# Optimization experiments

Hardware: AMD Instinct MI355X
Metric: run time of the kernel (lower is better)

The kernel has to match this reference:

```python
import jax, jax.numpy as jnp
import numpy as np

B, S, D, DH = 2, 2048, 1024, 64
H = D // DH
EPS = 1e-6

def rms_norm(x):
    # flax RMSNorm, use_scale=False: x / sqrt(mean(x^2) + eps)
    return x * jax.lax.rsqrt(jnp.mean(jnp.square(x), axis=-1, keepdims=True) + EPS)

def setup_inputs() -> dict:
    key = jax.random.key(0)
    ks = jax.random.split(key, 6)
    std = (1.0 / D) ** 0.5
    x = jax.random.normal(ks[0], (B, S, D), dtype=jnp.float32)
    Wq = jax.random.normal(ks[1], (D, D), dtype=jnp.float32) * std
    Wk = jax.random.normal(ks[2], (D, D), dtype=jnp.float32) * std
    Wv = jax.random.normal(ks[3], (D, D), dtype=jnp.float32) * std
    # output_proj is zero-initialized in the original; use small random so
    # backward through it is non-trivial for kernel correctness testing.
    Wo = jax.random.normal(ks[4], (D, D), dtype=jnp.float32) * std
    mask = jnp.tril(jnp.ones((S, S), dtype=bool))[None, None]  # causal [1,1,S,S]
    return {"x": x, "Wq": Wq, "Wk": Wk, "Wv": Wv, "Wo": Wo, "mask": mask}

def reference(x, Wq, Wk, Wv, Wo, mask):
    scale = (1.0 / DH) ** 0.5
    q = (x @ Wq).reshape(B, S, H, DH).transpose(0, 2, 1, 3)  # [B,H,S,DH]
    k = (x @ Wk).reshape(B, S, H, DH).transpose(0, 2, 1, 3)
    v = (x @ Wv).reshape(B, S, H, DH).transpose(0, 2, 1, 3)
    q = rms_norm(q)
    k = rms_norm(k)
    scores = jnp.einsum('bhsd,bhtd->bhst', q, k) * scale
    scores = jnp.where(mask, scores, jnp.finfo(scores.dtype).min)
    probs = jax.nn.softmax(scores, axis=-1)
    out = jnp.einsum('bhst,bhtd->bhsd', probs, v)
    out = out.transpose(0, 2, 1, 3).reshape(B, S, D)
    return out @ Wo
```

## Files before the change

### kernel.cpp

```cpp
#include <hip/hip_runtime.h>
#include <stdint.h>


typedef __attribute__((ext_vector_type(8))) short s16x8;
typedef __attribute__((ext_vector_type(4))) float fx4;
typedef __attribute__((ext_vector_type(4))) unsigned int ux4;
typedef __attribute__((ext_vector_type(2))) unsigned int ux2;

__device__ __forceinline__ unsigned short f2bf(float x) {
  unsigned u = __builtin_bit_cast(unsigned, x);
  u += 0x7fffu + ((u >> 16) & 1u);
  return (unsigned short)(u >> 16);
}
__device__ __forceinline__ float bf2f(unsigned short h) {
  return __builtin_bit_cast(float, (unsigned)h << 16);
}

__device__ __forceinline__ void gload_lds16(const void* g, void* l) {
  __builtin_amdgcn_global_load_lds(
      (const __attribute__((address_space(1))) unsigned int*)g,
      (__attribute__((address_space(3))) unsigned int*)l, 16, 0, 0);
}

__global__ void k_conv_bf16(const float* __restrict__ X,
                            unsigned short* __restrict__ Y, int n4) {
  int stride = gridDim.x * blockDim.x;
  for (int i = blockIdx.x * blockDim.x + threadIdx.x; i < n4; i += stride) {
    fx4 v = *(const fx4*)(X + (size_t)i * 4);
    ux2 o;
    o[0] = (unsigned)f2bf(v[0]) | ((unsigned)f2bf(v[1]) << 16);
    o[1] = (unsigned)f2bf(v[2]) | ((unsigned)f2bf(v[3]) << 16);
    *(ux2*)(Y + (size_t)i * 4) = o;
  }
}

__global__ void k_transpose_w(const float* __restrict__ W0, const float* __restrict__ W1,
                              const float* __restrict__ W2, const float* __restrict__ W3,
                              unsigned short* __restrict__ T0, unsigned short* __restrict__ T1,
                              unsigned short* __restrict__ T2, unsigned short* __restrict__ T3) {
  const float* W = blockIdx.z == 0 ? W0 : blockIdx.z == 1 ? W1 : blockIdx.z == 2 ? W2 : W3;
  unsigned short* T = blockIdx.z == 0 ? T0 : blockIdx.z == 1 ? T1 : blockIdx.z == 2 ? T2 : T3;
  __shared__ float t[32][33];
  int bx = blockIdx.x * 32, by = blockIdx.y * 32;
  int tx = threadIdx.x, ty = threadIdx.y;
#pragma unroll
  for (int i = 0; i < 32; i += 8)
    t[ty + i][tx] = W[(size_t)(by + ty + i) * 1024 + bx + tx];
  __syncthreads();
#pragma unroll
  for (int i = 0; i < 32; i += 8)
    T[(size_t)(bx + ty + i) * 1024 + by + tx] = f2bf(t[tx][ty + i]);
}

template <int MODE>
__global__ __launch_bounds__(256, 2)
void k_gemm_bt(const unsigned short* __restrict__ A,
               const unsigned short* __restrict__ W0,
               const unsigned short* __restrict__ W1,
               const unsigned short* __restrict__ W2,
               void* __restrict__ Cptr, int ldc,
               unsigned short* __restrict__ qn, unsigned short* __restrict__ kn,
               unsigned short* __restrict__ vb) {
  __shared__ unsigned short As[128 * 64];
  __shared__ unsigned short Bs[128 * 64];
  const int tid = threadIdx.x;
  const int w = tid >> 6, l = tid & 63;
  const int lr = l & 15, lg = l >> 4;
  const int wm = w >> 1, wn = w & 1;
  const int m0 = blockIdx.x * 128;
  const int nt = blockIdx.y;
  const unsigned short* Bt = (nt < 8) ? W0 : (nt < 16) ? W1 : W2;
  const int n0 = (nt & 7) * 128;

  fx4 acc[4][4] = {};

  const int srow = w * 8 + (l >> 3);
  const int skb  = ((l & 7) ^ (l >> 3)) * 8;
  const unsigned short* aB = A  + (size_t)(m0 + srow) * 1024 + skb;
  const unsigned short* bB = Bt + (size_t)(n0 + srow) * 1024 + skb;
  unsigned short* aD = &As[w * 512];
  unsigned short* bD = &Bs[w * 512];
  const int rdswz = (l & 7) << 4;

  for (int kt = 0; kt < 1024; kt += 64) {
    __syncthreads();
#pragma unroll
    for (int j = 0; j < 4; ++j) {
      gload_lds16(aB + j * 32768 + kt, aD + j * 2048);
      gload_lds16(bB + j * 32768 + kt, bD + j * 2048);
    }
    __syncthreads();
#pragma unroll
    for (int ks = 0; ks < 2; ++ks) {
      const int kb = (ks * 64 + lg * 16) ^ rdswz;
      s16x8 af[4], bf[4];
#pragma unroll
      for (int mf = 0; mf < 4; ++mf)
        af[mf] = *(const s16x8*)((const char*)As + (wm * 64 + mf * 16 + lr) * 128 + kb);
#pragma unroll
      for (int nf = 0; nf < 4; ++nf)
        bf[nf] = *(const s16x8*)((const char*)Bs + (wn * 64 + nf * 16 + lr) * 128 + kb);
#pragma unroll
      for (int mf = 0; mf < 4; ++mf)
#pragma unroll
        for (int nf = 0; nf < 4; ++nf)
          acc[mf][nf] = __builtin_amdgcn_mfma_f32_16x16x32_bf16(af[mf], bf[nf], acc[mf][nf], 0, 0, 0);
    }
  }

  if (MODE == 1) {
    const int gn = nt * 128 + wn * 64;
    const int gm = m0 + wm * 64;
#pragma unroll
    for (int mf = 0; mf < 4; ++mf)
#pragma unroll
      for (int r = 0; r < 4; ++r) {
        int row = gm + mf * 16 + lg * 4 + r;
        float* C = (float*)Cptr + (size_t)row * ldc + gn;
#pragma unroll
        for (int nf = 0; nf < 4; ++nf) C[nf * 16 + lr] = acc[mf][nf][r];
      }
  } else {
    const int tz = nt >> 3;
    const int h  = ((nt & 7) << 1) | wn;
    const int gm = m0 + wm * 64;
    unsigned short* base = tz == 0 ? qn : tz == 1 ? kn : vb;
    const float cmul = (tz == 0) ? 0.18033688f : 1.0f;
#pragma unroll
    for (int mf = 0; mf < 4; ++mf)
#pragma unroll
      for (int r = 0; r < 4; ++r) {
        int m = gm + mf * 16 + lg * 4 + r;
        float ss = 0.f;
#pragma unroll
        for (int nf = 0; nf < 4; ++nf) ss += acc[mf][nf][r] * acc[mf][nf][r];
        ss += __shfl_xor(ss, 1);
        ss += __shfl_xor(ss, 2);
        ss += __shfl_xor(ss, 4);
        ss += __shfl_xor(ss, 8);
        float scale = (tz == 2) ? 1.0f : rsqrtf(ss * (1.0f / 64.0f) + 1e-6f) * cmul;
        int b = m >> 11, s = m & 2047;
        unsigned short* dst = base + ((size_t)(((b << 4) + h) * 2048 + s)) * 64;
#pragma unroll
        for (int nf = 0; nf < 4; ++nf)
          dst[nf * 16 + lr] = f2bf(acc[mf][nf][r] * scale);
      }
  }
}

__global__ __launch_bounds__(256, 2)
void k_attn(const unsigned short* __restrict__ Q,
            const unsigned short* __restrict__ K,
            const unsigned short* __restrict__ V,
            unsigned short* __restrict__ O) {
  __shared__ unsigned short Ks[2][64 * 64];
  __shared__ unsigned short Vt[2][64 * 64];
  __shared__ unsigned short Ps[4][32 * 64];

  const int id = blockIdx.x;
  const int bh = id & 31;
  const int traw = id >> 5;
  const int tq = (traw < 8) ? traw : 23 - traw;
  const int q0 = tq * 128;
  const int tid = threadIdx.x;
  const int w = tid >> 6, l = tid & 63;
  const int lr = l & 15, lg = l >> 4;
  const int b = bh >> 4, h = bh & 15;
  const int qw = q0 + w * 32;

  const unsigned short* Kb = K + (size_t)bh * 2048 * 64;
  const unsigned short* Vb = V + (size_t)bh * 2048 * 64;
  const unsigned short* Qb = Q + ((size_t)bh * 2048 + qw) * 64;

  s16x8 aq[2][2];
#pragma unroll
  for (int mf = 0; mf < 2; ++mf)
#pragma unroll
    for (int ks = 0; ks < 2; ++ks)
      aq[mf][ks] = *(const s16x8*)(Qb + (mf * 16 + lr) * 64 + ks * 32 + lg * 8);

  fx4 oacc[2][4] = {};
  float lsum[2][4] = {{0.f, 0.f, 0.f, 0.f}, {0.f, 0.f, 0.f, 0.f}};

  const int ksrow = w * 8 + (l >> 3);
  const int kskb = ((l & 7) ^ (l >> 3)) * 8;
  const int vhalf = (tid & 31) >> 4;
  const int va_   = tid & 15;
  const int vdhg  = tid >> 5;
  const int vr0   = vhalf * 32 + va_;
  const int rdswz = (lr & 7) << 4;
  const float FMAX = 11.5415603f;

  const int ntl = 2 * (tq + 1);

  ux4 va0, va1;
#pragma unroll
  for (int j = 0; j < 2; ++j)
    gload_lds16(Kb + (size_t)(j * 32 + ksrow) * 64 + kskb, &Ks[0][j * 2048 + w * 512]);
  va0 = *(const ux4*)(Vb + (size_t)vr0 * 64 + vdhg * 8);
  va1 = *(const ux4*)(Vb + (size_t)(vr0 + 16) * 64 + vdhg * 8);
  {
    union { ux4 v; unsigned short u[8]; } a0, a1;
    a0.v = va0; a1.v = va1;
#pragma unroll
    for (int i = 0; i < 8; ++i) {
      int dh = vdhg * 8 + i;
      *(unsigned*)((char*)&Vt[0][0] + dh * 128 + ((vhalf * 64 + va_ * 4) ^ (i << 4))) =
          (unsigned)a0.u[i] | ((unsigned)a1.u[i] << 16);
    }
  }
  __syncthreads();

#pragma unroll 1
  for (int t = 0; t < ntl; ++t) {
    const int cur = t & 1;
    const int kv0 = t * 64;
    const bool pre = (t + 1 < ntl);
    if (pre) {
      const int kvn = kv0 + 64;
#pragma unroll
      for (int j = 0; j < 2; ++j)
        gload_lds16(Kb + (size_t)(kvn + j * 32 + ksrow) * 64 + kskb,
                    &Ks[cur ^ 1][j * 2048 + w * 512]);
      va0 = *(const ux4*)(Vb + (size_t)(kvn + vr0) * 64 + vdhg * 8);
      va1 = *(const ux4*)(Vb + (size_t)(kvn + vr0 + 16) * 64 + vdhg * 8);
    }
    if (kv0 <= qw + 31) {
      fx4 sc[2][4] = {};
#pragma unroll
      for (int ks = 0; ks < 2; ++ks) {
        const int kb = (ks * 64 + lg * 16) ^ rdswz;
#pragma unroll
        for (int nf = 0; nf < 4; ++nf) {
          s16x8 bk = *(const s16x8*)((const char*)&Ks[cur][0] + (nf * 16 + lr) * 128 + kb);
#pragma unroll
          for (int mf = 0; mf < 2; ++mf)
            sc[mf][nf] = __builtin_amdgcn_mfma_f32_16x16x32_bf16(aq[mf][ks], bk, sc[mf][nf], 0, 0, 0);
        }
      }
      if (kv0 + 63 > qw) {
#pragma unroll
        for (int mf = 0; mf < 2; ++mf)
#pragma unroll
          for (int nf = 0; nf < 4; ++nf)
#pragma unroll
            for (int r = 0; r < 4; ++r) {
              int gq = qw + mf * 16 + lg * 4 + r;
              int gk = kv0 + nf * 16 + lr;
              if (gk > gq) sc[mf][nf][r] = -3.0e38f;
            }
      }
      char* pw = (char*)&Ps[w][0];
#pragma unroll
      for (int mf = 0; mf < 2; ++mf)
#pragma unroll
        for (int r = 0; r < 4; ++r) {
          float p0 = __builtin_amdgcn_exp2f(sc[mf][0][r] - FMAX);
          float p1 = __builtin_amdgcn_exp2f(sc[mf][1][r] - FMAX);
          float p2 = __builtin_amdgcn_exp2f(sc[mf][2][r] - FMAX);
          float p3 = __builtin_amdgcn_exp2f(sc[mf][3][r] - FMAX);
          lsum[mf][r] += (p0 + p1) + (p2 + p3);
          int row = mf * 16 + lg * 4 + r;
          char* pb = pw + row * 128;
          int swz = (row & 7) << 4;
          *(unsigned*)(pb + ((4 * lr) ^ swz))      = (unsigned)f2bf(p0) | ((unsigned)f2bf(p1) << 16);
          *(unsigned*)(pb + ((64 + 4 * lr) ^ swz)) = (unsigned)f2bf(p2) | ((unsigned)f2bf(p3) << 16);
        }
#pragma unroll
      for (int ks = 0; ks < 2; ++ks) {
        s16x8 pa[2], bv[4];
#pragma unroll
        for (int mf = 0; mf < 2; ++mf) {
          int row = mf * 16 + lr;
          pa[mf] = *(const s16x8*)(pw + row * 128 + ((ks * 64 + lg * 16) ^ ((row & 7) << 4)));
        }
#pragma unroll
        for (int nf = 0; nf < 4; ++nf) {
          int row = nf * 16 + lr;
          bv[nf] = *(const s16x8*)((const char*)&Vt[cur][0] + row * 128 +
                                   ((ks * 64 + lg * 16) ^ ((row & 7) << 4)));
        }
#pragma unroll
        for (int mf = 0; mf < 2; ++mf)
#pragma unroll
          for (int nf = 0; nf < 4; ++nf)
            oacc[mf][nf] = __builtin_amdgcn_mfma_f32_16x16x32_bf16(pa[mf], bv[nf], oacc[mf][nf], 0, 0, 0);
      }
    }
    if (pre) {
      union { ux4 v; unsigned short u[8]; } a0, a1;
      a0.v = va0; a1.v = va1;
#pragma unroll
      for (int i = 0; i < 8; ++i) {
        int dh = vdhg * 8 + i;
        *(unsigned*)((char*)&Vt[cur ^ 1][0] + dh * 128 + ((vhalf * 64 + va_ * 4) ^ (i << 4))) =
            (unsigned)a0.u[i] | ((unsigned)a1.u[i] << 16);
      }
    }
    __syncthreads();
  }

#pragma unroll
  for (int mf = 0; mf < 2; ++mf)
#pragma unroll
    for (int r = 0; r < 4; ++r) {
      float s = lsum[mf][r];
      s += __shfl_xor(s, 1);
      s += __shfl_xor(s, 2);
      s += __shfl_xor(s, 4);
      s += __shfl_xor(s, 8);
      float inv = 1.0f / s;
      int gq = qw + mf * 16 + lg * 4 + r;
      unsigned short* orow = O + ((size_t)(b * 2048 + gq)) * 1024 + h * 64;
#pragma unroll
      for (int nf = 0; nf < 4; ++nf)
        orow[nf * 16 + lr] = f2bf(oacc[mf][nf][r] * inv);
    }
}

extern "C" void kernel_launch(void* const* d_in, const int* in_sizes, int n_in,
                              void* d_out, int out_size, void* d_ws, size_t ws_size,
                              hipStream_t stream) {
  const float* x  = (const float*)d_in[0];
  const float* Wq = (const float*)d_in[1];
  const float* Wk = (const float*)d_in[2];
  const float* Wv = (const float*)d_in[3];
  const float* Wo = (const float*)d_in[4];

  char* ws = (char*)d_ws;
  unsigned short* xb   = (unsigned short*)(ws);
  unsigned short* WqT  = (unsigned short*)(ws + (8ll  << 20));
  unsigned short* WkT  = (unsigned short*)(ws + (10ll << 20));
  unsigned short* WvT  = (unsigned short*)(ws + (12ll << 20));
  unsigned short* WoT  = (unsigned short*)(ws + (14ll << 20));
  unsigned short* qn   = (unsigned short*)(ws + (16ll << 20));
  unsigned short* kn   = (unsigned short*)(ws + (24ll << 20));
  unsigned short* vb   = (unsigned short*)(ws + (32ll << 20));
  unsigned short* attn = (unsigned short*)(ws + (40ll << 20));

  k_conv_bf16<<<1024, 256, 0, stream>>>(x, xb, 4096 * 1024 / 4);
  k_transpose_w<<<dim3(32, 32, 4), dim3(32, 8), 0, stream>>>(Wq, Wk, Wv, Wo, WqT, WkT, WvT, WoT);
  k_gemm_bt<2><<<dim3(32, 24), 256, 0, stream>>>(xb, WqT, WkT, WvT, nullptr, 0, qn, kn, vb);
  k_attn<<<512, 256, 0, stream>>>(qn, kn, vb, attn);
  k_gemm_bt<1><<<dim3(32, 8), 256, 0, stream>>>(attn, WoT, WoT, WoT, d_out, 1024, nullptr, nullptr, nullptr);
}
```

Before: 115.6 us.

## Split attention into 64-row query tiles with 2-wave blocks and balanced scheduling

The attention kernel now runs 1024 blocks of 128 threads, each covering 64 query rows instead of 128. Block order is interleaved so short and long causal tiles alternate, and the per-tile skip branch is removed because every KV tile up to the diagonal is now fully needed. s_setprio is raised around the MFMA sections, and the K/V staging is reshaped to suit two waves. Smaller blocks improve load balance and occupancy, at the cost of reloading K/V from global or L2 twice as often per query row.

```diff
diff --git a/kernel.cpp b/kernel.cpp
--- a/kernel.cpp
+++ b/kernel.cpp
@@ -148,20 +148,22 @@
   }
 }
 
-__global__ __launch_bounds__(256, 2)
+__global__ __launch_bounds__(128, 2)
 void k_attn(const unsigned short* __restrict__ Q,
             const unsigned short* __restrict__ K,
             const unsigned short* __restrict__ V,
             unsigned short* __restrict__ O) {
   __shared__ unsigned short Ks[2][64 * 64];
   __shared__ unsigned short Vt[2][64 * 64];
-  __shared__ unsigned short Ps[4][32 * 64];
+  __shared__ unsigned short Ps[2][32 * 64];
 
   const int id = blockIdx.x;
   const int bh = id & 31;
-  const int traw = id >> 5;
-  const int tq = (traw < 8) ? traw : 23 - traw;
-  const int q0 = tq * 128;
+  const int pp = id >> 5;
+  const int q2 = pp & 15;
+  const int bse = (q2 & 1) ? 15 - (q2 >> 1) : (q2 >> 1);
+  const int tq = (pp >> 4) ? 31 - bse : bse;
+  const int q0 = tq * 64;
   const int tid = threadIdx.x;
   const int w = tid >> 6, l = tid & 63;
   const int lr = l & 15, lg = l >> 4;
@@ -182,31 +184,34 @@
   fx4 oacc[2][4] = {};
   float lsum[2][4] = {{0.f, 0.f, 0.f, 0.f}, {0.f, 0.f, 0.f, 0.f}};
 
-  const int ksrow = w * 8 + (l >> 3);
-  const int kskb = ((l & 7) ^ (l >> 3)) * 8;
-  const int vhalf = (tid & 31) >> 4;
-  const int va_   = tid & 15;
-  const int vdhg  = tid >> 5;
-  const int vr0   = vhalf * 32 + va_;
+  const int ksub = l >> 3;
+  const int kskb = ((l & 7) ^ ksub) * 8;
+  const int vc = tid & 31;
+  const int vg = tid >> 5;
+  const int kvlo = (vc & 15) + (vc >> 4) * 32;
   const int rdswz = (lr & 7) << 4;
   const float FMAX = 11.5415603f;
-
-  const int ntl = 2 * (tq + 1);
-
-  ux4 va0, va1;
-#pragma unroll
-  for (int j = 0; j < 2; ++j)
-    gload_lds16(Kb + (size_t)(j * 32 + ksrow) * 64 + kskb, &Ks[0][j * 2048 + w * 512]);
-  va0 = *(const ux4*)(Vb + (size_t)vr0 * 64 + vdhg * 8);
-  va1 = *(const ux4*)(Vb + (size_t)(vr0 + 16) * 64 + vdhg * 8);
+  const int ntl = tq + 1;
+
+  ux4 va0, va1, va2, va3;
+#pragma unroll
+  for (int j = 0; j < 4; ++j)
+    gload_lds16(Kb + (size_t)(j * 16 + w * 8 + ksub) * 64 + kskb,
+                &Ks[0][(j * 16 + w * 8) * 64]);
+  va0 = *(const ux4*)(Vb + (size_t)kvlo * 64 + vg * 16);
+  va1 = *(const ux4*)(Vb + (size_t)kvlo * 64 + vg * 16 + 8);
+  va2 = *(const ux4*)(Vb + (size_t)(kvlo + 16) * 64 + vg * 16);
+  va3 = *(const ux4*)(Vb + (size_t)(kvlo + 16) * 64 + vg * 16 + 8);
   {
-    union { ux4 v; unsigned short u[8]; } a0, a1;
-    a0.v = va0; a1.v = va1;
+    union { ux4 v; unsigned short u[8]; } a0, a1, a2, a3;
+    a0.v = va0; a1.v = va1; a2.v = va2; a3.v = va3;
 #pragma unroll
     for (int i = 0; i < 8; ++i) {
-      int dh = vdhg * 8 + i;
-      *(unsigned*)((char*)&Vt[0][0] + dh * 128 + ((vhalf * 64 + va_ * 4) ^ (i << 4))) =
-          (unsigned)a0.u[i] | ((unsigned)a1.u[i] << 16);
+      int dh = vg * 16 + i;
+      *(unsigned*)((char*)&Vt[0][0] + dh * 128 + ((vc * 4) ^ ((i & 7) << 4))) =
+          (unsigned)a0.u[i] | ((unsigned)a2.u[i] << 16);
+      *(unsigned*)((char*)&Vt[0][0] + (dh + 8) * 128 + ((vc * 4) ^ ((i & 7) << 4))) =
+          (unsigned)a1.u[i] | ((unsigned)a3.u[i] << 16);
     }
   }
   __syncthreads();
@@ -219,82 +224,88 @@
     if (pre) {
       const int kvn = kv0 + 64;
 #pragma unroll
-      for (int j = 0; j < 2; ++j)
-        gload_lds16(Kb + (size_t)(kvn + j * 32 + ksrow) * 64 + kskb,
-                    &Ks[cur ^ 1][j * 2048 + w * 512]);
-      va0 = *(const ux4*)(Vb + (size_t)(kvn + vr0) * 64 + vdhg * 8);
-      va1 = *(const ux4*)(Vb + (size_t)(kvn + vr0 + 16) * 64 + vdhg * 8);
-    }
-    if (kv0 <= qw + 31) {
-      fx4 sc[2][4] = {};
-#pragma unroll
-      for (int ks = 0; ks < 2; ++ks) {
-        const int kb = (ks * 64 + lg * 16) ^ rdswz;
-#pragma unroll
-        for (int nf = 0; nf < 4; ++nf) {
-          s16x8 bk = *(const s16x8*)((const char*)&Ks[cur][0] + (nf * 16 + lr) * 128 + kb);
-#pragma unroll
-          for (int mf = 0; mf < 2; ++mf)
-            sc[mf][nf] = __builtin_amdgcn_mfma_f32_16x16x32_bf16(aq[mf][ks], bk, sc[mf][nf], 0, 0, 0);
-        }
-      }
-      if (kv0 + 63 > qw) {
+      for (int j = 0; j < 4; ++j)
+        gload_lds16(Kb + (size_t)(kvn + j * 16 + w * 8 + ksub) * 64 + kskb,
+                    &Ks[cur ^ 1][(j * 16 + w * 8) * 64]);
+      va0 = *(const ux4*)(Vb + (size_t)(kvn + kvlo) * 64 + vg * 16);
+      va1 = *(const ux4*)(Vb + (size_t)(kvn + kvlo) * 64 + vg * 16 + 8);
+      va2 = *(const ux4*)(Vb + (size_t)(kvn + kvlo + 16) * 64 + vg * 16);
+      va3 = *(const ux4*)(Vb + (size_t)(kvn + kvlo + 16) * 64 + vg * 16 + 8);
+    }
+    fx4 sc[2][4] = {};
+    __builtin_amdgcn_s_setprio(1);
+#pragma unroll
+    for (int ks = 0; ks < 2; ++ks) {
+      const int kb = (ks * 64 + lg * 16) ^ rdswz;
+#pragma unroll
+      for (int nf = 0; nf < 4; ++nf) {
+        s16x8 bk = *(const s16x8*)((const char*)&Ks[cur][0] + (nf * 16 + lr) * 128 + kb);
 #pragma unroll
         for (int mf = 0; mf < 2; ++mf)
-#pragma unroll
-          for (int nf = 0; nf < 4; ++nf)
-#pragma unroll
-            for (int r = 0; r < 4; ++r) {
-              int gq = qw + mf * 16 + lg * 4 + r;
-              int gk = kv0 + nf * 16 + lr;
-              if (gk > gq) sc[mf][nf][r] = -3.0e38f;
-            }
-      }
-      char* pw = (char*)&Ps[w][0];
+          sc[mf][nf] = __builtin_amdgcn_mfma_f32_16x16x32_bf16(aq[mf][ks], bk, sc[mf][nf], 0, 0, 0);
+      }
+    }
+    __builtin_amdgcn_s_setprio(0);
+    if (t == ntl - 1) {
 #pragma unroll
       for (int mf = 0; mf < 2; ++mf)
 #pragma unroll
-        for (int r = 0; r < 4; ++r) {
-          float p0 = __builtin_amdgcn_exp2f(sc[mf][0][r] - FMAX);
-          float p1 = __builtin_amdgcn_exp2f(sc[mf][1][r] - FMAX);
-          float p2 = __builtin_amdgcn_exp2f(sc[mf][2][r] - FMAX);
-          float p3 = __builtin_amdgcn_exp2f(sc[mf][3][r] - FMAX);
-          lsum[mf][r] += (p0 + p1) + (p2 + p3);
-          int row = mf * 16 + lg * 4 + r;
-          char* pb = pw + row * 128;
-          int swz = (row & 7) << 4;
-          *(unsigned*)(pb + ((4 * lr) ^ swz))      = (unsigned)f2bf(p0) | ((unsigned)f2bf(p1) << 16);
-          *(unsigned*)(pb + ((64 + 4 * lr) ^ swz)) = (unsigned)f2bf(p2) | ((unsigned)f2bf(p3) << 16);
-        }
-#pragma unroll
-      for (int ks = 0; ks < 2; ++ks) {
-        s16x8 pa[2], bv[4];
-#pragma unroll
-        for (int mf = 0; mf < 2; ++mf) {
-          int row = mf * 16 + lr;
-          pa[mf] = *(const s16x8*)(pw + row * 128 + ((ks * 64 + lg * 16) ^ ((row & 7) << 4)));
-        }
-#pragma unroll
-        for (int nf = 0; nf < 4; ++nf) {
-          int row = nf * 16 + lr;
-          bv[nf] = *(const s16x8*)((const char*)&Vt[cur][0] + row * 128 +
-                                   ((ks * 64 + lg * 16) ^ ((row & 7) << 4)));
-        }
-#pragma unroll
-        for (int mf = 0; mf < 2; ++mf)
-#pragma unroll
-          for (int nf = 0; nf < 4; ++nf)
-            oacc[mf][nf] = __builtin_amdgcn_mfma_f32_16x16x32_bf16(pa[mf], bv[nf], oacc[mf][nf], 0, 0, 0);
-      }
-    }
+        for (int nf = 0; nf < 4; ++nf)
+#pragma unroll
+          for (int r = 0; r < 4; ++r) {
+            int gq = qw + mf * 16 + lg * 4 + r;
+            int gk = kv0 + nf * 16 + lr;
+            if (gk > gq) sc[mf][nf][r] = -3.0e38f;
+          }
+    }
+    char* pw = (char*)&Ps[w][0];
+#pragma unroll
+    for (int mf = 0; mf < 2; ++mf)
+#pragma unroll
+      for (int r = 0; r < 4; ++r) {
+        float p0 = __builtin_amdgcn_exp2f(sc[mf][0][r] - FMAX);
+        float p1 = __builtin_amdgcn_exp2f(sc[mf][1][r] - FMAX);
+        float p2 = __builtin_amdgcn_exp2f(sc[mf][2][r] - FMAX);
+        float p3 = __builtin_amdgcn_exp2f(sc[mf][3][r] - FMAX);
+        lsum[mf][r] += (p0 + p1) + (p2 + p3);
+        int row = mf * 16 + lg * 4 + r;
+        char* pb = pw + row * 128;
+        int swz = (row & 7) << 4;
+        *(unsigned*)(pb + ((4 * lr) ^ swz))      = (unsigned)f2bf(p0) | ((unsigned)f2bf(p1) << 16);
+        *(unsigned*)(pb + ((64 + 4 * lr) ^ swz)) = (unsigned)f2bf(p2) | ((unsigned)f2bf(p3) << 16);
+      }
+    __builtin_amdgcn_s_setprio(1);
+#pragma unroll
+    for (int ks = 0; ks < 2; ++ks) {
+      s16x8 pa[2], bv[4];
+#pragma unroll
+      for (int mf = 0; mf < 2; ++mf) {
+        int row = mf * 16 + lr;
+        pa[mf] = *(const s16x8*)(pw + row * 128 + ((ks * 64 + lg * 16) ^ ((row & 7) << 4)));
+      }
+#pragma unroll
+      for (int nf = 0; nf < 4; ++nf) {
+        int row = nf * 16 + lr;
+        bv[nf] = *(const s16x8*)((const char*)&Vt[cur][0] + row * 128 +
+                                 ((ks * 64 + lg * 16) ^ ((row & 7) << 4)));
+      }
+#pragma unroll
+      for (int mf = 0; mf < 2; ++mf)
+#pragma unroll
+        for (int nf = 0; nf < 4; ++nf)
+          oacc[mf][nf] = __builtin_amdgcn_mfma_f32_16x16x32_bf16(pa[mf], bv[nf], oacc[mf][nf], 0, 0, 0);
+    }
+    __builtin_amdgcn_s_setprio(0);
     if (pre) {
-      union { ux4 v; unsigned short u[8]; } a0, a1;
-      a0.v = va0; a1.v = va1;
+      union { ux4 v; unsigned short u[8]; } a0, a1, a2, a3;
+      a0.v = va0; a1.v = va1; a2.v = va2; a3.v = va3;
 #pragma unroll
       for (int i = 0; i < 8; ++i) {
-        int dh = vdhg * 8 + i;
-        *(unsigned*)((char*)&Vt[cur ^ 1][0] + dh * 128 + ((vhalf * 64 + va_ * 4) ^ (i << 4))) =
-            (unsigned)a0.u[i] | ((unsigned)a1.u[i] << 16);
+        int dh = vg * 16 + i;
+        *(unsigned*)((char*)&Vt[cur ^ 1][0] + dh * 128 + ((vc * 4) ^ ((i & 7) << 4))) =
+            (unsigned)a0.u[i] | ((unsigned)a2.u[i] << 16);
+        *(unsigned*)((char*)&Vt[cur ^ 1][0] + (dh + 8) * 128 + ((vc * 4) ^ ((i & 7) << 4))) =
+            (unsigned)a1.u[i] | ((unsigned)a3.u[i] << 16);
       }
     }
     __syncthreads();
@@ -341,6 +352,6 @@
   k_conv_bf16<<<1024, 256, 0, stream>>>(x, xb, 4096 * 1024 / 4);
   k_transpose_w<<<dim3(32, 32, 4), dim3(32, 8), 0, stream>>>(Wq, Wk, Wv, Wo, WqT, WkT, WvT, WoT);
   k_gemm_bt<2><<<dim3(32, 24), 256, 0, stream>>>(xb, WqT, WkT, WvT, nullptr, 0, qn, kn, vb);
-  k_attn<<<512, 256, 0, stream>>>(qn, kn, vb, attn);
+  k_attn<<<1024, 128, 0, stream>>>(qn, kn, vb, attn);
   k_gemm_bt<1><<<dim3(32, 8), 256, 0, stream>>>(attn, WoT, WoT, WoT, d_out, 1024, nullptr, nullptr, nullptr);
 }
```

Result: no change. 117.9 us (+2.0%).
